# Performance work log

Hardware: AMD Instinct MI355X
Metric: run time of the kernel (lower is better)

The kernel has to match this reference:

```python
import jax, jax.numpy as jnp
import numpy as np

N = 512      # hidden_size
L = 16384    # sequence length


def _make_hippo_legs(n_dim):
    # make_HiPPO_legs from the source
    b = jnp.sqrt(1.0 + 2.0 * jnp.arange(n_dim, dtype=jnp.float32))
    a = b[:, None] * b[None, :]
    a = jnp.tril(a) - jnp.diag(jnp.arange(n_dim, dtype=jnp.float32))
    return -a, b


def setup_inputs() -> dict:
    key = jax.random.key(0)
    c_key, x_key = jax.random.split(key, 2)
    A, Bv = _make_hippo_legs(N)
    B = Bv[:, None]                                   # (N, 1)
    C = jax.random.normal(c_key, (1, N), dtype=jnp.float32)
    in_x = jax.random.normal(x_key, (L,), dtype=jnp.float32)
    hidden_state = jnp.zeros((N,), dtype=jnp.float32)
    return {"in_x": in_x, "hidden_state": hidden_state, "A": A, "B": B, "C": C}


def reference(in_x, hidden_state, A, B, C):
    # discretize (bilinear / Tustin) with step = 1/L
    step = 1.0 / in_x.shape[0]
    I = jnp.eye(A.shape[0], dtype=A.dtype)
    BL = jnp.linalg.inv(I - (step / 2.0) * A)
    Ab = BL @ (I + (step / 2.0) * A)                  # (N, N)
    Bb = (BL * step) @ B                              # (N, 1)

    def step_through_time(h, x):
        # x: (1,) ; h: (N,)
        h_new = Ab @ h + Bb @ x                       # (N,)
        return h_new, C @ h_new                      # output (1,)

    new_hidden_state, output = jax.lax.scan(step_through_time, hidden_state, in_x[:, None])
    return output.squeeze(), new_hidden_state
```

## Files before the change

### kernel.cpp

```cpp
#include <hip/hip_runtime.h>

#define NDIM 512
#define LSEQ 16384
#define TCH  1024
#define PCH  16

#define DTF  (1.0f/16384.0f)
#define DT2F (0.5f/16384.0f)

__device__ __forceinline__ void gkt(float* smem,
    const float* A, int lda, const float* B, int ldb,
    float* D, int ldd, int row0, int col0, int K, float alpha)
{
    const int tid  = threadIdx.x;
    const int w    = tid >> 6;
    const int lane = tid & 63;
    const int ty = lane >> 3, tx = lane & 7;

    float* As = smem + w * 1152;
    float* Bs = As + 576;

    const int Kc    = K >> 2;
    const int steps = Kc >> 4;
    const int kbase = w * Kc;

    float acc[4][4] = {};

    for (int s = 0; s < steps; ++s) {
        const int kb = kbase + s * 16;
#pragma unroll
        for (int i = 0; i < 2; ++i) {
            int idx = lane + 64 * i;
            int r = idx >> 2, cg2 = (idx & 3) * 4;
            float4 v = *(const float4*)(A + (size_t)(row0 + r) * lda + kb + cg2);
            As[(cg2 + 0) * 36 + r] = v.x; As[(cg2 + 1) * 36 + r] = v.y;
            As[(cg2 + 2) * 36 + r] = v.z; As[(cg2 + 3) * 36 + r] = v.w;
        }
#pragma unroll
        for (int i = 0; i < 2; ++i) {
            int idx = lane + 64 * i;
            int kr = idx >> 3, cg2 = (idx & 7) * 4;
            *(float4*)(Bs + kr * 36 + cg2) =
                *(const float4*)(B + (size_t)(kb + kr) * ldb + col0 + cg2);
        }
        __syncthreads();
#pragma unroll
        for (int kk = 0; kk < 16; ++kk) {
            float4 a = *(const float4*)(As + kk * 36 + 4 * ty);
            float4 b = *(const float4*)(Bs + kk * 36 + 4 * tx);
            acc[0][0] += a.x * b.x; acc[0][1] += a.x * b.y; acc[0][2] += a.x * b.z; acc[0][3] += a.x * b.w;
            acc[1][0] += a.y * b.x; acc[1][1] += a.y * b.y; acc[1][2] += a.y * b.z; acc[1][3] += a.y * b.w;
            acc[2][0] += a.z * b.x; acc[2][1] += a.z * b.y; acc[2][2] += a.z * b.z; acc[2][3] += a.z * b.w;
            acc[3][0] += a.w * b.x; acc[3][1] += a.w * b.y; acc[3][2] += a.w * b.z; acc[3][3] += a.w * b.w;
        }
        __syncthreads();
    }

    float* red = smem + w * 1152;
#pragma unroll
    for (int i = 0; i < 4; ++i)
        *(float4*)(red + (4 * ty + i) * 32 + 4 * tx) =
            make_float4(acc[i][0], acc[i][1], acc[i][2], acc[i][3]);
    __syncthreads();

    float4 s0 = *(const float4*)(smem + 0 * 1152 + tid * 4);
    float4 s1 = *(const float4*)(smem + 1 * 1152 + tid * 4);
    float4 s2 = *(const float4*)(smem + 2 * 1152 + tid * 4);
    float4 s3 = *(const float4*)(smem + 3 * 1152 + tid * 4);
    float4 r4 = make_float4(alpha * (s0.x + s1.x + s2.x + s3.x),
                            alpha * (s0.y + s1.y + s2.y + s3.y),
                            alpha * (s0.z + s1.z + s2.z + s3.z),
                            alpha * (s0.w + s1.w + s2.w + s3.w));
    int r = tid >> 3, c = (tid & 7) * 4;
    float* dp = D + (size_t)(row0 + r) * ldd + col0 + c;
    dp[0] = r4.x; dp[1] = r4.y; dp[2] = r4.z; dp[3] = r4.w;
}

__device__ __forceinline__ void tri_decode(int t, int& it, int& jt)
{
    it = (int)((sqrtf(8.f * (float)t + 1.f) - 1.f) * 0.5f);
    while ((it + 1) * (it + 2) / 2 <= t) ++it;
    while (it * (it + 1) / 2 > t) --it;
    jt = t - it * (it + 1) / 2;
}

__global__ __launch_bounds__(64) void diag_inv(const float* __restrict__ A,
                                               float* __restrict__ W)
{
    __shared__ float sh[64][65];
    const int base = blockIdx.x * 64;
    const int lane = threadIdx.x;

    for (int r = 0; r < 64; ++r)
        sh[r][lane] = ((r == lane) ? 1.f : 0.f)
                    - DT2F * A[(size_t)(base + r) * NDIM + base + lane];
    __syncthreads();

    float xcol[64];
#pragma unroll
    for (int i = 0; i < 64; ++i) {
        float dot = 0.f;
#pragma unroll
        for (int k = 0; k < i; ++k) dot += sh[i][k] * xcol[k];
        xcol[i] = (((lane == i) ? 1.f : 0.f) - dot) / sh[i][i];
    }
#pragma unroll
    for (int k = 0; k < 64; ++k)
        W[(size_t)(base + k) * NDIM + base + lane] = xcol[k];
}

__global__ __launch_bounds__(256) void pairA2(const float* __restrict__ A,
    const float* __restrict__ W, float* __restrict__ T, int s)
{
    __shared__ float smem[4608];
    int ntx = s >> 5;
    int tile = blockIdx.x;
    int it = tile / ntx, jt = tile - it * ntx;
    int o = blockIdx.y * 2 * s;
    int col0 = jt * 32, k0 = col0 & ~63;
    gkt(smem, A + (size_t)(o + s) * NDIM + o + k0, NDIM,
        W + (size_t)(o + k0) * NDIM + o, NDIM,
        T + (size_t)(o + s) * NDIM + o, NDIM,
        it * 32, col0, s - k0, 1.f);
}

__global__ __launch_bounds__(256) void pairB2(float* __restrict__ W,
    const float* __restrict__ T, int s)
{
    __shared__ float smem[4608];
    int ntx = s >> 5;
    int tile = blockIdx.x;
    int it = tile / ntx, jt = tile - it * ntx;
    int o = blockIdx.y * 2 * s;
    int ke = (it * 32 + 32 + 63) & ~63; if (ke > s) ke = s;
    gkt(smem, W + (size_t)(o + s) * NDIM + (o + s), NDIM,
        T + (size_t)(o + s) * NDIM + o, NDIM,
        W + (size_t)(o + s) * NDIM + o, NDIM,
        it * 32, jt * 32, ke, DT2F);
}

__global__ __launch_bounds__(256) void form_prep(const float* __restrict__ W,
    const float* __restrict__ Bv, const float* __restrict__ C,
    float* __restrict__ Ab, float* __restrict__ V, float* __restrict__ Crows,
    float* __restrict__ Bbc)
{
    const int b = blockIdx.x, tid = threadIdx.x;
    if (b < 256) {
        int idx = b * 256 + tid;
        int i = idx >> 7, j0 = (idx & 127) << 2;
        float4 wq = *(const float4*)(W + (size_t)i * NDIM + j0);
        float4 r = make_float4(2.f * wq.x, 2.f * wq.y, 2.f * wq.z, 2.f * wq.w);
        if (i == j0)          r.x -= 1.f;
        else if (i == j0 + 1) r.y -= 1.f;
        else if (i == j0 + 2) r.z -= 1.f;
        else if (i == j0 + 3) r.w -= 1.f;
        *(float4*)(Ab + (size_t)i * NDIM + j0) = r;
    } else if (b < 384) {
        const int wv = tid >> 6, lane = tid & 63;
        int i = (b - 256) * 4 + wv;
        float s = 0.f;
        int rmax = i >> 6;
        for (int c = 0; c <= rmax; ++c) {
            int k = (c << 6) + lane;
            if (k <= i) s += W[(size_t)i * NDIM + k] * Bv[k];
        }
#pragma unroll
        for (int off = 32; off; off >>= 1) s += __shfl_xor(s, off, 64);
        if (lane == 0) {
            float bb = DTF * s;
            V[(size_t)i * TCH] = bb;
            Bbc[i] = bb;
        }
    } else {
        Crows[tid]       = C[tid];
        Crows[tid + 256] = C[tid + 256];
    }
}

__global__ __launch_bounds__(256) void round_kernel(const float* __restrict__ g,
    float* __restrict__ gnew, float* __restrict__ V, float* __restrict__ Crows,
    int m, int lognx)
{
    __shared__ float smem[4608];
    const int z = blockIdx.z;
    const int tile_id = blockIdx.y * 16 + blockIdx.x;
    if (z == 2) {
        if (tile_id >= 136) return;
        int it, jt;
        tri_decode(tile_id, it, jt);
        int k0 = (jt * 32) & ~63;
        int ke = (it * 32 + 32 + 63) & ~63; if (ke > NDIM) ke = NDIM;
        gkt(smem, g + k0, NDIM, g + (size_t)k0 * NDIM, NDIM,
            gnew, NDIM, it * 32, jt * 32, ke - k0, 1.f);
    } else if (z == 0) {
        if (m >= TCH) return;
        int nmx = (m >= 32) ? (m >> 5) : 1;
        if (tile_id >= (nmx << 4)) return;
        int it = tile_id >> lognx, jt = tile_id & (nmx - 1);
        int ke = (it * 32 + 32 + 63) & ~63; if (ke > NDIM) ke = NDIM;
        gkt(smem, g, NDIM, V, TCH, V + m, TCH, it * 32, jt * 32, ke, 1.f);
    } else {
        if (m >= TCH) return;
        int nty = (m >= 32) ? (m >> 5) : 1;
        if (tile_id >= (nty << 4)) return;
        int it = tile_id >> 4, jt = tile_id & 15;
        int col0 = jt * 32, k0 = col0 & ~63;
        gkt(smem, Crows + k0, NDIM, g + (size_t)k0 * NDIM, NDIM,
            Crows + (size_t)m * NDIM, NDIM, it * 32, col0, NDIM - k0, 1.f);
    }
}

__global__ __launch_bounds__(256) void cb_kernel(
    const float* __restrict__ Crows, const float* __restrict__ Ab,
    float* __restrict__ CrowsS, const float* __restrict__ Bbc,
    float* __restrict__ kv, const float* __restrict__ V,
    const float* __restrict__ x, const float* __restrict__ GA,
    const float* __restrict__ hs, float* __restrict__ U)
{
    const int t = blockIdx.x;
    const int wv = threadIdx.x >> 6, lane = threadIdx.x & 63;
    if (t < 512) {
        __shared__ float smem[4608];
        int it = t >> 4, jt = t & 15;
        int col0 = jt * 32, k0 = col0 & ~63;
        gkt(smem, Crows + k0, NDIM, Ab + (size_t)k0 * NDIM, NDIM,
            CrowsS, NDIM, it * 32, col0, NDIM - k0, 1.f);
    } else if (t < 768) {
        int j = (t - 512) * 4 + wv;
        const float* cr = Crows + (size_t)j * NDIM;
        float dot = 0.f;
#pragma unroll
        for (int rr = 0; rr < 2; ++rr) {
            int o = rr * 256 + lane * 4;
            float4 c4 = *(const float4*)(cr + o);
            float4 b4 = *(const float4*)(Bbc + o);
            dot += c4.x * b4.x + c4.y * b4.y + c4.z * b4.z + c4.w * b4.w;
        }
#pragma unroll
        for (int off = 32; off; off >>= 1) dot += __shfl_xor(dot, off, 64);
        if (lane == 0) kv[j] = dot;
    } else {
        int wid = (t - 768) * 4 + wv;
        int p = wid & (PCH - 1), i = wid >> 4;
        const float* vr = V + (size_t)i * TCH;
        const float* xc = x + p * TCH;
        float s = 0.f;
#pragma unroll
        for (int rr = 0; rr < 16; ++rr) {
            int t2 = (rr << 6) + lane;
            s += vr[TCH - 1 - t2] * xc[t2];
        }
        if (p == 0) {
            const float* gr = GA + (size_t)i * NDIM;
            int rmax = i >> 6;
            for (int rr = 0; rr <= rmax; ++rr) {
                int k = (rr << 6) + lane;
                if (k <= i) s += gr[k] * hs[k];
            }
        }
#pragma unroll
        for (int off = 32; off; off >>= 1) s += __shfl_xor(s, off, 64);
        if (lane == 0) U[(size_t)p * NDIM + i] = s;
    }
}

__global__ __launch_bounds__(256) void scan_round(const float* __restrict__ G,
    const float* __restrict__ Zold, float* __restrict__ Znew,
    const float* __restrict__ hs, float* __restrict__ Hmat,
    float* __restrict__ hfin, int o, int last)
{
    int wid = blockIdx.x * 4 + (threadIdx.x >> 6);
    int lane = threadIdx.x & 63;
    int p = wid & (PCH - 1), i = wid >> 4;
    float dot = 0.f;
    if (p >= o) {
        const float* gr = G + (size_t)i * NDIM;
        const float* zc = Zold + (size_t)(p - o) * NDIM;
        int rmax = i >> 6;
        for (int r = 0; r <= rmax; ++r) {
            int k = (r << 6) + lane;
            if (k <= i) dot += gr[k] * zc[k];
        }
#pragma unroll
        for (int off = 32; off; off >>= 1) dot += __shfl_xor(dot, off, 64);
    }
    if (lane == 0) {
        float z = Zold[(size_t)p * NDIM + i] + dot;
        Znew[(size_t)p * NDIM + i] = z;
        if (last) {
            if (p < PCH - 1) Hmat[(size_t)(p + 1) * NDIM + i] = z;
            else hfin[i] = z;
            if (p == 0) Hmat[i] = hs[i];
        }
    }
}

__global__ __launch_bounds__(256) void emit(const float* __restrict__ CrowsS,
    const float* __restrict__ Hmat, const float* __restrict__ kv,
    const float* __restrict__ x, float* __restrict__ out)
{
    int wid = blockIdx.x * 4 + (threadIdx.x >> 6);
    int lane = threadIdx.x & 63;
    int p = wid & (PCH - 1), s = wid >> 4;
    const float* cr = CrowsS + (size_t)s * NDIM;
    const float* hp = Hmat + (size_t)p * NDIM;
    float dot = 0.f;
#pragma unroll
    for (int r = 0; r < 2; ++r) {
        int o = r * 256 + lane * 4;
        float4 c = *(const float4*)(cr + o);
        float4 h = *(const float4*)(hp + o);
        dot += c.x * h.x + c.y * h.y + c.z * h.z + c.w * h.w;
    }
    const float* xc = x + p * TCH;
    int rmax = s >> 6;
    for (int r = 0; r <= rmax; ++r) {
        int t = (r << 6) + lane;
        if (t <= s) dot += kv[s - t] * xc[t];
    }
#pragma unroll
    for (int off = 32; off; off >>= 1) dot += __shfl_xor(dot, off, 64);
    if (lane == 0) out[p * TCH + s] = dot;
}

extern "C" void kernel_launch(void* const* d_in, const int* in_sizes, int n_in,
                              void* d_out, int out_size, void* d_ws, size_t ws_size,
                              hipStream_t stream)
{
    (void)in_sizes; (void)n_in; (void)out_size; (void)ws_size;
    const float* x  = (const float*)d_in[0];
    const float* hs = (const float*)d_in[1];
    const float* A  = (const float*)d_in[2];
    const float* Bv = (const float*)d_in[3];
    const float* C  = (const float*)d_in[4];
    float* out = (float*)d_out;

    const int MM = NDIM * NDIM;
    float* ws     = (float*)d_ws;
    float* Ab     = ws;
    float* P0     = Ab + MM;
    float* P1     = P0 + MM;
    float* GA     = P1 + MM;
    float* GB     = GA + MM;
    float* GC     = GB + MM;
    float* GD     = GC + MM;
    float* V      = GD + MM;
    float* Crows  = V + NDIM * TCH;
    float* CrowsS = Crows + TCH * NDIM;
    float* kv     = CrowsS + TCH * NDIM;
    float* Bbc    = kv + TCH;
    float* U      = Bbc + NDIM;
    float* Z0     = U + PCH * NDIM;
    float* Z1     = Z0 + PCH * NDIM;
    float* Hmat   = Z1 + PCH * NDIM;

    float* W = CrowsS;
    float* T = P0;

    hipMemsetAsync(W, 0, MM * sizeof(float), stream);
    hipMemsetAsync(P0, 0, (size_t)6 * MM * sizeof(float), stream);

    diag_inv<<<8, 64, 0, stream>>>(A, W);
    for (int s = 64; s <= 256; s <<= 1) {
        int np = NDIM / (2 * s);
        int tiles = (s >> 5) * (s >> 5);
        dim3 grid(tiles, np);
        pairA2<<<grid, 256, 0, stream>>>(A, W, T, s);
        pairB2<<<grid, 256, 0, stream>>>(W, T, s);
    }
    form_prep<<<385, 256, 0, stream>>>(W, Bv, C, Ab, V, Crows, Bbc);

    const float* g = Ab;
    float* gouts[13] = {P0, P1, P0, P1, P0, P1, P0, P1, P0, GA, GB, GC, GD};
    int m = 1;
    for (int r = 0; r < 13; ++r) {
        int lognx = (r >= 5) ? (r - 5) : 0;
        round_kernel<<<dim3(16, 16, 3), 256, 0, stream>>>(g, gouts[r], V, Crows,
                                                          m, lognx);
        g = gouts[r];
        m <<= 1;
    }

    cb_kernel<<<2816, 256, 0, stream>>>(Crows, Ab, CrowsS, Bbc, kv, V, x, GA,
                                        hs, U);

    scan_round<<<2048, 256, 0, stream>>>(GA, U,  Z0, hs, Hmat, out + LSEQ, 1, 0);
    scan_round<<<2048, 256, 0, stream>>>(GB, Z0, Z1, hs, Hmat, out + LSEQ, 2, 0);
    scan_round<<<2048, 256, 0, stream>>>(GC, Z1, Z0, hs, Hmat, out + LSEQ, 4, 0);
    scan_round<<<2048, 256, 0, stream>>>(GD, Z0, Z1, hs, Hmat, out + LSEQ, 8, 1);

    emit<<<4096, 256, 0, stream>>>(CrowsS, Hmat, kv, x, out);
}
```

Before: 305.7 us.

## Fuse tail stages into squaring rounds and replace memsets with targeted zeroing

```diff
diff --git a/kernel.cpp b/kernel.cpp
--- a/kernel.cpp
+++ b/kernel.cpp
@@ -84,29 +84,71 @@
     jt = t - it * (it + 1) / 2;
 }
 
-__global__ __launch_bounds__(64) void diag_inv(const float* __restrict__ A,
-                                               float* __restrict__ W)
+__device__ __forceinline__ void scan_task(int task, const float* G,
+    const float* Zold, float* Znew, const float* hs, float* Hmat,
+    float* hfin, int o, int last)
+{
+    int wid = task * 4 + (threadIdx.x >> 6);
+    int lane = threadIdx.x & 63;
+    int p = wid & (PCH - 1), i = wid >> 4;
+    float dot = 0.f;
+    if (p >= o) {
+        const float* gr = G + (size_t)i * NDIM;
+        const float* zc = Zold + (size_t)(p - o) * NDIM;
+        int rmax = i >> 6;
+        for (int r = 0; r <= rmax; ++r) {
+            int k = (r << 6) + lane;
+            if (k <= i) dot += gr[k] * zc[k];
+        }
+#pragma unroll
+        for (int off = 32; off; off >>= 1) dot += __shfl_xor(dot, off, 64);
+    }
+    if (lane == 0) {
+        float z = Zold[(size_t)p * NDIM + i] + dot;
+        Znew[(size_t)p * NDIM + i] = z;
+        if (last) {
+            if (p < PCH - 1) Hmat[(size_t)(p + 1) * NDIM + i] = z;
+            else hfin[i] = z;
+            if (p == 0) Hmat[i] = hs[i];
+        }
+    }
+}
+
+__global__ __launch_bounds__(256) void zero_diag(const float* __restrict__ A,
+    float* __restrict__ W, float* __restrict__ P0)
 {
     __shared__ float sh[64][65];
-    const int base = blockIdx.x * 64;
-    const int lane = threadIdx.x;
-
-    for (int r = 0; r < 64; ++r)
-        sh[r][lane] = ((r == lane) ? 1.f : 0.f)
-                    - DT2F * A[(size_t)(base + r) * NDIM + base + lane];
-    __syncthreads();
-
-    float xcol[64];
-#pragma unroll
-    for (int i = 0; i < 64; ++i) {
-        float dot = 0.f;
-#pragma unroll
-        for (int k = 0; k < i; ++k) dot += sh[i][k] * xcol[k];
-        xcol[i] = (((lane == i) ? 1.f : 0.f) - dot) / sh[i][i];
-    }
-#pragma unroll
-    for (int k = 0; k < 64; ++k)
-        W[(size_t)(base + k) * NDIM + base + lane] = xcol[k];
+    const int t = blockIdx.x, tid = threadIdx.x;
+    if (t < 8) {
+        const int base = t * 64;
+        for (int idx = tid; idx < 4096; idx += 256) {
+            int r = idx >> 6, c = idx & 63;
+            sh[r][c] = ((r == c) ? 1.f : 0.f)
+                     - DT2F * A[(size_t)(base + r) * NDIM + base + c];
+        }
+        __syncthreads();
+        if (tid < 64) {
+            const int lane = tid;
+            float xcol[64];
+#pragma unroll
+            for (int i = 0; i < 64; ++i) {
+                float dot = 0.f;
+#pragma unroll
+                for (int k = 0; k < i; ++k) dot += sh[i][k] * xcol[k];
+                xcol[i] = (((lane == i) ? 1.f : 0.f) - dot) / sh[i][i];
+            }
+#pragma unroll
+            for (int k = 0; k < 64; ++k)
+                W[(size_t)(base + k) * NDIM + base + lane] = xcol[k];
+        }
+    } else {
+        const int q = (t - 8) >> 3, d = (t - 8) & 7;
+        float* buf = P0 + (size_t)q * NDIM * NDIM;
+        for (int idx = tid; idx < 4096; idx += 256) {
+            int r = idx >> 6, c = idx & 63;
+            if (c > r) buf[(size_t)(d * 64 + r) * NDIM + d * 64 + c] = 0.f;
+        }
+    }
 }
 
 __global__ __launch_bounds__(256) void pairA2(const float* __restrict__ A,
@@ -132,7 +174,7 @@
     int tile = blockIdx.x;
     int it = tile / ntx, jt = tile - it * ntx;
     int o = blockIdx.y * 2 * s;
-    int ke = (it * 32 + 32 + 63) & ~63; if (ke > s) ke = s;
+    int ke = (it * 32 + 95) & ~63; if (ke > s) ke = s;
     gkt(smem, W + (size_t)(o + s) * NDIM + (o + s), NDIM,
         T + (size_t)(o + s) * NDIM + o, NDIM,
         W + (size_t)(o + s) * NDIM + o, NDIM,
@@ -177,90 +219,100 @@
     }
 }
 
-__global__ __launch_bounds__(256) void round_kernel(const float* __restrict__ g,
-    float* __restrict__ gnew, float* __restrict__ V, float* __restrict__ Crows,
-    int m, int lognx)
+__global__ __launch_bounds__(256) void round_kernel(
+    const float* __restrict__ g, float* __restrict__ gnew,
+    float* __restrict__ V, float* __restrict__ Crows,
+    int m, int lognx, int nz, int tailmode,
+    const float* __restrict__ Gscan, const float* __restrict__ Ab,
+    const float* __restrict__ x, const float* __restrict__ hs,
+    const float* __restrict__ Bbc, float* __restrict__ kv,
+    float* __restrict__ U, const float* __restrict__ Zin,
+    float* __restrict__ Zout, float* __restrict__ Hmat,
+    float* __restrict__ hfin, int o)
 {
     __shared__ float smem[4608];
-    const int z = blockIdx.z;
-    const int tile_id = blockIdx.y * 16 + blockIdx.x;
-    if (z == 2) {
-        if (tile_id >= 136) return;
+    const int t = blockIdx.x;
+    const int tid = threadIdx.x;
+    const int wv = tid >> 6, lane = tid & 63;
+
+    if (t < 136) {
         int it, jt;
-        tri_decode(tile_id, it, jt);
+        tri_decode(t, it, jt);
         int k0 = (jt * 32) & ~63;
-        int ke = (it * 32 + 32 + 63) & ~63; if (ke > NDIM) ke = NDIM;
+        int ke = (it * 32 + 95) & ~63; if (ke > NDIM) ke = NDIM;
         gkt(smem, g + k0, NDIM, g + (size_t)k0 * NDIM, NDIM,
             gnew, NDIM, it * 32, jt * 32, ke - k0, 1.f);
-    } else if (z == 0) {
-        if (m >= TCH) return;
+        return;
+    }
+    int u = t - 136;
+    if (tailmode == 0) {
         int nmx = (m >= 32) ? (m >> 5) : 1;
-        if (tile_id >= (nmx << 4)) return;
-        int it = tile_id >> lognx, jt = tile_id & (nmx - 1);
-        int ke = (it * 32 + 32 + 63) & ~63; if (ke > NDIM) ke = NDIM;
-        gkt(smem, g, NDIM, V, TCH, V + m, TCH, it * 32, jt * 32, ke, 1.f);
+        if (u < nz) {
+            int it = u >> lognx, jt = u & (nmx - 1);
+            int ke = (it * 32 + 95) & ~63; if (ke > NDIM) ke = NDIM;
+            gkt(smem, g, NDIM, V, TCH, V + m, TCH, it * 32, jt * 32, ke, 1.f);
+        } else {
+            u -= nz;
+            int it = u >> 4, jt = u & 15;
+            int col0 = jt * 32, k0 = col0 & ~63;
+            gkt(smem, Crows + k0, NDIM, g + (size_t)k0 * NDIM, NDIM,
+                Crows + (size_t)m * NDIM, NDIM, it * 32, col0, NDIM - k0, 1.f);
+        }
+    } else if (tailmode == 1) {
+        if (u < 2) {
+            float* cs = smem;
+            for (int k = tid; k < NDIM; k += 256)
+                cs[k] = Crows[(size_t)1023 * NDIM + k];
+            __syncthreads();
+            int j = u * 256 + tid;
+            int k0 = j & ~63;
+            float acc = 0.f;
+            for (int k = k0; k < NDIM; k += 4) {
+                acc += cs[k]     * Ab[(size_t)k * NDIM + j]
+                     + cs[k + 1] * Ab[(size_t)(k + 1) * NDIM + j]
+                     + cs[k + 2] * Ab[(size_t)(k + 2) * NDIM + j]
+                     + cs[k + 3] * Ab[(size_t)(k + 3) * NDIM + j];
+            }
+            Crows[(size_t)1024 * NDIM + j] = acc;
+        } else if (u < 258) {
+            int j = (u - 2) * 4 + wv;
+            const float* cr = Crows + (size_t)j * NDIM;
+            float dot = 0.f;
+#pragma unroll
+            for (int rr = 0; rr < 2; ++rr) {
+                int oo = rr * 256 + lane * 4;
+                float4 c4 = *(const float4*)(cr + oo);
+                float4 b4 = *(const float4*)(Bbc + oo);
+                dot += c4.x * b4.x + c4.y * b4.y + c4.z * b4.z + c4.w * b4.w;
+            }
+#pragma unroll
+            for (int off = 32; off; off >>= 1) dot += __shfl_xor(dot, off, 64);
+            if (lane == 0) kv[j] = dot;
+        } else {
+            int wid = (u - 258) * 4 + wv;
+            int p = wid & (PCH - 1), i = wid >> 4;
+            const float* vr = V + (size_t)i * TCH;
+            const float* xc = x + p * TCH;
+            float s = 0.f;
+#pragma unroll
+            for (int rr = 0; rr < 16; ++rr) {
+                int t2 = (rr << 6) + lane;
+                s += vr[TCH - 1 - t2] * xc[t2];
+            }
+            if (p == 0) {
+                const float* gr = Gscan + (size_t)i * NDIM;
+                int rmax = i >> 6;
+                for (int rr = 0; rr <= rmax; ++rr) {
+                    int k = (rr << 6) + lane;
+                    if (k <= i) s += gr[k] * hs[k];
+                }
+            }
+#pragma unroll
+            for (int off = 32; off; off >>= 1) s += __shfl_xor(s, off, 64);
+            if (lane == 0) U[(size_t)p * NDIM + i] = s;
+        }
     } else {
-        if (m >= TCH) return;
-        int nty = (m >= 32) ? (m >> 5) : 1;
-        if (tile_id >= (nty << 4)) return;
-        int it = tile_id >> 4, jt = tile_id & 15;
-        int col0 = jt * 32, k0 = col0 & ~63;
-        gkt(smem, Crows + k0, NDIM, g + (size_t)k0 * NDIM, NDIM,
-            Crows + (size_t)m * NDIM, NDIM, it * 32, col0, NDIM - k0, 1.f);
-    }
-}
-
-__global__ __launch_bounds__(256) void cb_kernel(
-    const float* __restrict__ Crows, const float* __restrict__ Ab,
-    float* __restrict__ CrowsS, const float* __restrict__ Bbc,
-    float* __restrict__ kv, const float* __restrict__ V,
-    const float* __restrict__ x, const float* __restrict__ GA,
-    const float* __restrict__ hs, float* __restrict__ U)
-{
-    const int t = blockIdx.x;
-    const int wv = threadIdx.x >> 6, lane = threadIdx.x & 63;
-    if (t < 512) {
-        __shared__ float smem[4608];
-        int it = t >> 4, jt = t & 15;
-        int col0 = jt * 32, k0 = col0 & ~63;
-        gkt(smem, Crows + k0, NDIM, Ab + (size_t)k0 * NDIM, NDIM,
-            CrowsS, NDIM, it * 32, col0, NDIM - k0, 1.f);
-    } else if (t < 768) {
-        int j = (t - 512) * 4 + wv;
-        const float* cr = Crows + (size_t)j * NDIM;
-        float dot = 0.f;
-#pragma unroll
-        for (int rr = 0; rr < 2; ++rr) {
-            int o = rr * 256 + lane * 4;
-            float4 c4 = *(const float4*)(cr + o);
-            float4 b4 = *(const float4*)(Bbc + o);
-            dot += c4.x * b4.x + c4.y * b4.y + c4.z * b4.z + c4.w * b4.w;
-        }
-#pragma unroll
-        for (int off = 32; off; off >>= 1) dot += __shfl_xor(dot, off, 64);
-        if (lane == 0) kv[j] = dot;
-    } else {
-        int wid = (t - 768) * 4 + wv;
-        int p = wid & (PCH - 1), i = wid >> 4;
-        const float* vr = V + (size_t)i * TCH;
-        const float* xc = x + p * TCH;
-        float s = 0.f;
-#pragma unroll
-        for (int rr = 0; rr < 16; ++rr) {
-            int t2 = (rr << 6) + lane;
-            s += vr[TCH - 1 - t2] * xc[t2];
-        }
-        if (p == 0) {
-            const float* gr = GA + (size_t)i * NDIM;
-            int rmax = i >> 6;
-            for (int rr = 0; rr <= rmax; ++rr) {
-                int k = (rr << 6) + lane;
-                if (k <= i) s += gr[k] * hs[k];
-            }
-        }
-#pragma unroll
-        for (int off = 32; off; off >>= 1) s += __shfl_xor(s, off, 64);
-        if (lane == 0) U[(size_t)p * NDIM + i] = s;
+        scan_task(u, Gscan, Zin, Zout, hs, Hmat, hfin, o, 0);
     }
 }
 
@@ -269,40 +321,17 @@
     const float* __restrict__ hs, float* __restrict__ Hmat,
     float* __restrict__ hfin, int o, int last)
 {
-    int wid = blockIdx.x * 4 + (threadIdx.x >> 6);
-    int lane = threadIdx.x & 63;
-    int p = wid & (PCH - 1), i = wid >> 4;
-    float dot = 0.f;
-    if (p >= o) {
-        const float* gr = G + (size_t)i * NDIM;
-        const float* zc = Zold + (size_t)(p - o) * NDIM;
-        int rmax = i >> 6;
-        for (int r = 0; r <= rmax; ++r) {
-            int k = (r << 6) + lane;
-            if (k <= i) dot += gr[k] * zc[k];
-        }
-#pragma unroll
-        for (int off = 32; off; off >>= 1) dot += __shfl_xor(dot, off, 64);
-    }
-    if (lane == 0) {
-        float z = Zold[(size_t)p * NDIM + i] + dot;
-        Znew[(size_t)p * NDIM + i] = z;
-        if (last) {
-            if (p < PCH - 1) Hmat[(size_t)(p + 1) * NDIM + i] = z;
-            else hfin[i] = z;
-            if (p == 0) Hmat[i] = hs[i];
-        }
-    }
-}
-
-__global__ __launch_bounds__(256) void emit(const float* __restrict__ CrowsS,
+    scan_task(blockIdx.x, G, Zold, Znew, hs, Hmat, hfin, o, last);
+}
+
+__global__ __launch_bounds__(256) void emit(const float* __restrict__ Crows,
     const float* __restrict__ Hmat, const float* __restrict__ kv,
     const float* __restrict__ x, float* __restrict__ out)
 {
     int wid = blockIdx.x * 4 + (threadIdx.x >> 6);
     int lane = threadIdx.x & 63;
     int p = wid & (PCH - 1), s = wid >> 4;
-    const float* cr = CrowsS + (size_t)s * NDIM;
+    const float* cr = Crows + (size_t)(s + 1) * NDIM;
     const float* hp = Hmat + (size_t)p * NDIM;
     float dot = 0.f;
 #pragma unroll
@@ -346,21 +375,19 @@
     float* GD     = GC + MM;
     float* V      = GD + MM;
     float* Crows  = V + NDIM * TCH;
-    float* CrowsS = Crows + TCH * NDIM;
-    float* kv     = CrowsS + TCH * NDIM;
+    float* CrowsW = Crows + TCH * NDIM;
+    float* kv     = CrowsW + TCH * NDIM;
     float* Bbc    = kv + TCH;
     float* U      = Bbc + NDIM;
     float* Z0     = U + PCH * NDIM;
     float* Z1     = Z0 + PCH * NDIM;
     float* Hmat   = Z1 + PCH * NDIM;
 
-    float* W = CrowsS;
+    float* W = CrowsW;
     float* T = P0;
 
-    hipMemsetAsync(W, 0, MM * sizeof(float), stream);
-    hipMemsetAsync(P0, 0, (size_t)6 * MM * sizeof(float), stream);
-
-    diag_inv<<<8, 64, 0, stream>>>(A, W);
+    zero_diag<<<56, 256, 0, stream>>>(A, W, P0);
+
     for (int s = 64; s <= 256; s <<= 1) {
         int np = NDIM / (2 * s);
         int tiles = (s >> 5) * (s >> 5);
@@ -374,20 +401,24 @@
     float* gouts[13] = {P0, P1, P0, P1, P0, P1, P0, P1, P0, GA, GB, GC, GD};
     int m = 1;
     for (int r = 0; r < 13; ++r) {
+        int nmx = (m >= 32) ? (m >> 5) : 1;
         int lognx = (r >= 5) ? (r - 5) : 0;
-        round_kernel<<<dim3(16, 16, 3), 256, 0, stream>>>(g, gouts[r], V, Crows,
-                                                          m, lognx);
+        int nz = (m < TCH) ? 16 * nmx : 0;
+        int tailmode = 0, ntail = 0, oo = 0;
+        const float* Gs = GA; const float* Zi = U; float* Zo = Z0;
+        if (r == 10)      { tailmode = 1; ntail = 2306; }
+        else if (r == 11) { tailmode = 2; ntail = 2048; oo = 1; }
+        else if (r == 12) { tailmode = 2; ntail = 2048; oo = 2; Gs = GB;
+                            Zi = Z0; Zo = Z1; }
+        round_kernel<<<136 + 2 * nz + ntail, 256, 0, stream>>>(
+            g, gouts[r], V, Crows, m, lognx, nz, tailmode, Gs, Ab,
+            x, hs, Bbc, kv, U, Zi, Zo, Hmat, out + LSEQ, oo);
         g = gouts[r];
         m <<= 1;
     }
 
-    cb_kernel<<<2816, 256, 0, stream>>>(Crows, Ab, CrowsS, Bbc, kv, V, x, GA,
-                                        hs, U);
-
-    scan_round<<<2048, 256, 0, stream>>>(GA, U,  Z0, hs, Hmat, out + LSEQ, 1, 0);
-    scan_round<<<2048, 256, 0, stream>>>(GB, Z0, Z1, hs, Hmat, out + LSEQ, 2, 0);
     scan_round<<<2048, 256, 0, stream>>>(GC, Z1, Z0, hs, Hmat, out + LSEQ, 4, 0);
     scan_round<<<2048, 256, 0, stream>>>(GD, Z0, Z1, hs, Hmat, out + LSEQ, 8, 1);
 
-    emit<<<4096, 256, 0, stream>>>(CrowsS, Hmat, kv, x, out);
-}
+    emit<<<4096, 256, 0, stream>>>(Crows, Hmat, kv, x, out);
+}
```

Result: no change. 311.2 us (+1.8%).
